# Kernel optimization log

Measured on AMD Instinct MI355X. Metric: run time of the kernel, lower is better.

The kernel has to match this reference:

```python
import jax, jax.numpy as jnp
import numpy as np

B, NPB, F = 8, 8192, 64          # clouds, points/cloud, feature dim
RATIO, R, K, C = 0.25, 0.1, 32, 128
M = int(NPB * RATIO)             # 2048 sampled points per cloud


def setup_inputs() -> dict:
    key = jax.random.key(0)
    k1, k2, k3, k4 = jax.random.split(key, 4)
    x = jax.random.normal(k1, (B * NPB, F), dtype=jnp.float32)
    pos = jax.random.uniform(k2, (B * NPB, 3), dtype=jnp.float32)
    batch = (jnp.arange(B * NPB) // NPB).astype(jnp.int32)
    W1 = jax.random.normal(k3, (F + 3, C), dtype=jnp.float32) * (1.0 / np.sqrt(F + 3))
    b1 = jax.random.normal(k4, (C,), dtype=jnp.float32) * 0.01
    return {"x": x, "pos": pos, "batch": batch, "W1": W1, "b1": b1}


def _fps(pos_b):
    # Farthest point sampling on one cloud [NPB,3] -> [M] indices.
    # Deterministic start at index 0 (random_start=False, eval mode).
    dmin0 = jnp.full((NPB,), jnp.inf, dtype=pos_b.dtype)
    def step(carry, _):
        dmin, last = carry
        d = jnp.sum((pos_b - pos_b[last]) ** 2, axis=-1)
        dmin = jnp.minimum(dmin, d)
        nxt = jnp.argmax(dmin).astype(jnp.int32)
        return (dmin, nxt), last
    (_, _), idx = jax.lax.scan(step, (dmin0, jnp.int32(0)), None, length=M)
    return idx


def reference(x, pos, batch, W1, b1):
    posb = pos.reshape(B, NPB, 3)
    xb = x.reshape(B, NPB, F)

    samp = jax.vmap(_fps)(posb)                                   # [B,M] per-cloud idx
    qpos = jnp.take_along_axis(posb, samp[..., None], axis=1)     # [B,M,3]

    # radius ball query: up to K nearest within R (self always included, d=0)
    d2 = jnp.sum((qpos[:, :, None, :] - posb[:, None, :, :]) ** 2, axis=-1)  # [B,M,NPB]
    score = jnp.where(d2 <= R * R, -d2, -jnp.inf)
    vals, nbr = jax.lax.top_k(score, K)                           # [B,M,K]
    valid = vals > -jnp.inf

    flat = nbr.reshape(B, M * K)
    nbr_pos = jnp.take_along_axis(posb, flat[..., None], axis=1).reshape(B, M, K, 3)
    nbr_x = jnp.take_along_axis(xb, flat[..., None], axis=1).reshape(B, M, K, F)

    # PointNet conv: MLP on [x_j, pos_j - pos_i], max-aggregate over neighbors
    msg_in = jnp.concatenate([nbr_x, nbr_pos - qpos[:, :, None, :]], axis=-1)  # [B,M,K,F+3]
    h = jax.nn.relu(jnp.einsum('bmkf,fc->bmkc', msg_in, W1) + b1)
    h = jnp.where(valid[..., None], h, -jnp.inf)
    out = jnp.max(h, axis=2)                                      # [B,M,C]

    idx_global = (samp + (jnp.arange(B, dtype=jnp.int32) * NPB)[:, None]).reshape(-1)
    return (out.reshape(B * M, C),
            qpos.reshape(B * M, 3),
            jnp.take(batch, idx_global),
            idx_global)
```

## Files before the change

kernel.cpp:

```cpp
#include <hip/hip_runtime.h>

#define NPB 8192
#define NB 8
#define MQ 2048
#define FD 64
#define KN 32
#define CD 128
#define NQ (NB*MQ)
#define CAP 512
#define NCB 248
#define NUNITS (NCB*4)
#define UPC (NUNITS/NB)
#define QITERS ((MQ + UPC - 1) / UPC)
#define PSTRIDE 16

typedef unsigned long long ull;
typedef float v2f __attribute__((ext_vector_type(2)));

#define LDS_BARRIER() asm volatile("s_waitcnt lgkmcnt(0)\n\ts_barrier" ::: "memory")

__device__ __forceinline__ float dist2(float ax, float ay, float az,
                                       float bx, float by, float bz) {
    float dx = __fsub_rn(ax, bx);
    float dy = __fsub_rn(ay, by);
    float dz = __fsub_rn(az, bz);
    return __fadd_rn(__fadd_rn(__fmul_rn(dx, dx), __fmul_rn(dy, dy)), __fmul_rn(dz, dz));
}

__device__ __forceinline__ double key_as_f64(ull k) {
    return __longlong_as_double((long long)k);
}
__device__ __forceinline__ ull key_as_u64(double d) {
    return (ull)__double_as_longlong(d);
}

template <int CTRL>
__device__ __forceinline__ double dpp_max_f64_step(double key) {
    ull u = key_as_u64(key);
    int lo = (int)(unsigned)u, hi = (int)(u >> 32);
    int lo2 = __builtin_amdgcn_update_dpp(0, lo, CTRL, 0xf, 0xf, false);
    int hi2 = __builtin_amdgcn_update_dpp(0, hi, CTRL, 0xf, 0xf, false);
    double o = key_as_f64(((ull)(unsigned)hi2 << 32) | (unsigned)lo2);
    return fmax(key, o);
}

__device__ __forceinline__ double dpp_max_f64(double key) {
    key = dpp_max_f64_step<0x111>(key);
    key = dpp_max_f64_step<0x112>(key);
    key = dpp_max_f64_step<0x114>(key);
    key = dpp_max_f64_step<0x118>(key);
    key = dpp_max_f64_step<0x142>(key);
    key = dpp_max_f64_step<0x143>(key);
    return key;
}

__device__ __forceinline__ double dpp_max_f64_groups8(double key) {
    key = dpp_max_f64_step<0x118>(key);
    key = dpp_max_f64_step<0x142>(key);
    key = dpp_max_f64_step<0x143>(key);
    return key;
}

__device__ __forceinline__ unsigned morton9(float x, float y, float z) {
    unsigned cx = (unsigned)min(7, max(0, (int)(x * 8.0f)));
    unsigned cy = (unsigned)min(7, max(0, (int)(y * 8.0f)));
    unsigned cz = (unsigned)min(7, max(0, (int)(z * 8.0f)));
    return (cx & 1) | ((cy & 1) << 1) | ((cz & 1) << 2)
         | ((cx & 2) << 2) | ((cy & 2) << 3) | ((cz & 2) << 4)
         | ((cx & 4) << 4) | ((cy & 4) << 5) | ((cz & 4) << 6);
}

struct FpsSlot {
    ull key;
    float x, y, z;
    float pad[3];
};
struct FpsSM {
    float2 sxy[NPB];
    float sz[NPB];
    unsigned sidx[NPB];
    __align__(16) FpsSlot slot[2][8];
    unsigned hist[512];
    unsigned off[512];
};
struct UnitSM {
    float msg[KN][68];
    ull buf[CAP];
    int nb[KN];
    int scnt;
    int pad;
};
union SMU {
    FpsSM f;
    UnitSM u[4];
};

__global__ __launch_bounds__(512) void mega_kernel(const float* __restrict__ xin,
                                                   const float* __restrict__ pos,
                                                   const float* __restrict__ W1,
                                                   const float* __restrict__ b1,
                                                   int* __restrict__ samp,
                                                   int* __restrict__ progress,
                                                   float* __restrict__ out) {
    __shared__ SMU sm;
    const int tid = threadIdx.x;

    if (blockIdx.x < NB) {
        const int b = blockIdx.x;
        const int wv = tid >> 6, lane = tid & 63;
        const float* p0 = pos + (size_t)b * NPB * 3;

        sm.f.hist[tid] = 0;
        __syncthreads();
        for (int i = tid; i < NPB; i += 512) {
            float x = p0[i * 3 + 0];
            float y = p0[i * 3 + 1];
            float z = p0[i * 3 + 2];
            sm.f.sxy[i] = make_float2(x, y);
            sm.f.sz[i] = z;
            atomicAdd(&sm.f.hist[morton9(x, y, z)], 1);
        }
        __syncthreads();

        if (tid < 8) {
            FpsSlot* d = &sm.f.slot[1][tid];
            d->key = ((ull)0x7f800000u << 32) | 0xFFFFFFFFu;
            d->x = sm.f.sxy[0].x;
            d->y = sm.f.sxy[0].y;
            d->z = sm.f.sz[0];
        }

        unsigned hval = sm.f.hist[tid];
        unsigned* src = sm.f.hist;
        unsigned* dst = sm.f.off;
        #pragma unroll 1
        for (int d = 1; d < 512; d <<= 1) {
            unsigned v = src[tid];
            if (tid >= d) v += src[tid - d];
            __syncthreads();
            dst[tid] = v;
            __syncthreads();
            unsigned* tmp = src; src = dst; dst = tmp;
        }
        unsigned excl = src[tid] - hval;
        dst[tid] = excl;
        unsigned* cursor = dst;
        __syncthreads();

        for (int i = tid; i < NPB; i += 512) {
            float2 xy = sm.f.sxy[i];
            unsigned m = morton9(xy.x, xy.y, sm.f.sz[i]);
            unsigned p = atomicAdd(&cursor[m], 1);
            sm.f.sidx[p] = (unsigned)i;
        }
        __syncthreads();

        const int perm8[8] = {0, 1, 2, 3, 7, 6, 5, 4};
        const unsigned* sp = &sm.f.sidx[perm8[wv] * 1024 + lane * 16];
        v2f px2[8], py2[8], pz2[8], dmin2[8];
        unsigned norig[16];
        const float inf = __builtin_huge_valf();
        float bx0 = inf, bx1 = -inf;
        float by0 = inf, by1 = -inf;
        float bz0 = inf, bz1 = -inf;
        #pragma unroll
        for (int i = 0; i < 8; i++) {
            unsigned o0 = sp[2 * i + 0];
            unsigned o1 = sp[2 * i + 1];
            norig[2 * i + 0] = ~o0;
            norig[2 * i + 1] = ~o1;
            float2 a = sm.f.sxy[o0], c2 = sm.f.sxy[o1];
            float za = sm.f.sz[o0], zc = sm.f.sz[o1];
            px2[i] = (v2f){a.x, c2.x};
            py2[i] = (v2f){a.y, c2.y};
            pz2[i] = (v2f){za, zc};
            dmin2[i] = (v2f){inf, inf};
            bx0 = fminf(bx0, fminf(a.x, c2.x)); bx1 = fmaxf(bx1, fmaxf(a.x, c2.x));
            by0 = fminf(by0, fminf(a.y, c2.y)); by1 = fmaxf(by1, fmaxf(a.y, c2.y));
            bz0 = fminf(bz0, fminf(za, zc));    bz1 = fmaxf(bz1, fmaxf(za, zc));
        }
        double mykey = key_as_f64((ull)0x7f800000u << 32);
        ull cachedkey = 0;
        float cachedx = 0.f, cachedy = 0.f, cachedz = 0.f;
        __syncthreads();

        for (int t = 0; t < MQ; t++) {
            const FpsSlot* srd = &sm.f.slot[(t - 1) & 1][lane >> 3];
            ulonglong2 rv = *(const ulonglong2*)srd;
            float gzf = srd->z;
            ull kg = rv.x;
            double krd = dpp_max_f64_groups8(key_as_f64(kg));
            ull krb = key_as_u64(krd);
            unsigned whi = (unsigned)__builtin_amdgcn_readlane((int)(krb >> 32), 63);
            unsigned wlo = (unsigned)__builtin_amdgcn_readlane((int)(unsigned)krb, 63);
            ull wk = ((ull)whi << 32) | wlo;
            int last = (int)((~wlo) & (NPB - 1));
            ull iswin = __ballot(kg == wk);
            int wl = __ffsll((long long)iswin) - 1;
            int gxi = (int)(unsigned)rv.y;
            int gyi = (int)(rv.y >> 32);
            float lx = __int_as_float(__builtin_amdgcn_readlane(gxi, wl));
            float ly = __int_as_float(__builtin_amdgcn_readlane(gyi, wl));
            float lz = __int_as_float(__builtin_amdgcn_readlane(__float_as_int(gzf), wl));

            if (tid == 448) {
                samp[b * MQ + t] = last;
                if ((t & 15) == 15)
                    __hip_atomic_store(&progress[b * PSTRIDE], t + 1, __ATOMIC_RELEASE,
                                       __HIP_MEMORY_SCOPE_AGENT);
            }

            float ddx = fmaxf(fmaxf(bx0 - lx, lx - bx1), 0.0f);
            float ddy = fmaxf(fmaxf(by0 - ly, ly - by1), 0.0f);
            float ddz = fmaxf(fmaxf(bz0 - lz, lz - bz1), 0.0f);
            float dlb = ddx * ddx + ddy * ddy + ddz * ddz;
            float cm = __uint_as_float((unsigned)(key_as_u64(mykey) >> 32));
            bool act = __fmul_rn(0.999f, dlb) < cm;

            if (__any(act)) {
                if (act) {
                    #pragma clang fp contract(off)
                    double ba = 0.0, bb = 0.0;
                    #pragma unroll
                    for (int i = 0; i < 8; i++) {
                        v2f dx = px2[i] - lx;
                        v2f dy = py2[i] - ly;
                        v2f dz = pz2[i] - lz;
                        v2f d2v = (dx * dx + dy * dy) + dz * dz;
                        float d0 = fminf(dmin2[i].x, d2v.x);
                        float d1 = fminf(dmin2[i].y, d2v.y);
                        dmin2[i] = (v2f){d0, d1};
                        double k0 = key_as_f64(((ull)__float_as_uint(d0) << 32) | norig[2 * i + 0]);
                        double k1 = key_as_f64(((ull)__float_as_uint(d1) << 32) | norig[2 * i + 1]);
                        ba = fmax(ba, k0);
                        bb = fmax(bb, k1);
                    }
                    mykey = fmax(ba, bb);
                }
                double w = dpp_max_f64(mykey);
                ull wb = key_as_u64(w);
                unsigned chi = (unsigned)__builtin_amdgcn_readlane((int)(wb >> 32), 63);
                unsigned clo = (unsigned)__builtin_amdgcn_readlane((int)(unsigned)wb, 63);
                cachedkey = ((ull)chi << 32) | clo;
                int wi = (int)((~clo) & (NPB - 1));
                float2 cxy = sm.f.sxy[wi];
                cachedx = cxy.x;
                cachedy = cxy.y;
                cachedz = sm.f.sz[wi];
            }
            if (lane == 63) {
                FpsSlot* d = &sm.f.slot[t & 1][wv];
                ulonglong2 wv2;
                wv2.x = cachedkey;
                wv2.y = ((ull)(unsigned)__float_as_int(cachedy) << 32)
                      | (unsigned)__float_as_int(cachedx);
                *(ulonglong2*)d = wv2;
                d->z = cachedz;
            }
            LDS_BARRIER();
        }
        return;
    }

    const int c = blockIdx.x - NB;
    const int unit = tid >> 7;
    const int ut = tid & 127;
    UnitSM& U = sm.u[unit];
    const int g = c * 4 + unit;
    const int b = g & 7;
    const int ui = g >> 3;
    const float RR = (float)(0.1 * 0.1);
    const float* P = pos + (size_t)b * NPB * 3;

    float w[68];
    #pragma unroll
    for (int f = 0; f < 67; f++) w[f] = W1[f * CD + ut];
    w[67] = 0.0f;
    const float bias = b1[ut];

    for (int r = 0; r < QITERS; r++) {
        const int tq = r * UPC + ui;
        const bool active = tq < MQ;
        const int q = (b << 11) + tq;
        int s = 0;
        float qx = 0.f, qy = 0.f, qz = 0.f;

        if (active && ut == 0) {
            while (__hip_atomic_load(&progress[b * PSTRIDE], __ATOMIC_RELAXED,
                                     __HIP_MEMORY_SCOPE_AGENT) < tq + 1) {}
            __builtin_amdgcn_fence(__ATOMIC_ACQUIRE, "agent");
            U.scnt = 0;
        }
        __syncthreads();

        if (active) {
            s = samp[q] & (NPB - 1);
            qx = P[s * 3 + 0]; qy = P[s * 3 + 1]; qz = P[s * 3 + 2];
            for (int p = ut; p < NPB; p += 128) {
                float xx = P[p * 3 + 0];
                float yy = P[p * 3 + 1];
                float zz = P[p * 3 + 2];
                float d2v = dist2(qx, qy, qz, xx, yy, zz);
                if (d2v <= RR) {
                    int slot = atomicAdd(&U.scnt, 1);
                    if (slot < CAP)
                        U.buf[slot] = ((ull)__float_as_uint(d2v) << 32) | (unsigned)p;
                }
            }
        }
        __syncthreads();

        int n = 0, nk = 0;
        if (active) {
            n = U.scnt; if (n > CAP) n = CAP;
            nk = (n < KN) ? n : KN;
        }
        if (active && ut < 64) {
            if (n <= 64) {
                ull key = (ut < n) ? U.buf[ut] : ~0ULL;
                #pragma unroll
                for (int k = 2; k <= 64; k <<= 1) {
                    #pragma unroll
                    for (int j = k >> 1; j > 0; j >>= 1) {
                        ull o = __shfl_xor(key, (unsigned)j, 64);
                        bool ascending = ((ut & k) == 0);
                        bool upper = ((ut & j) != 0);
                        bool keepMin = (ascending != upper);
                        ull mn = (o < key) ? o : key;
                        ull mx = (o < key) ? key : o;
                        key = keepMin ? mn : mx;
                    }
                }
                if (ut < nk) U.nb[ut] = ((int)(unsigned)key) & (NPB - 1);
            } else {
                ull ck[CAP / 64];
                #pragma unroll
                for (int i = 0; i < CAP / 64; i++) {
                    int sl = ut + i * 64;
                    ck[i] = (sl < n) ? U.buf[sl] : ~0ULL;
                }
                for (int rr = 0; rr < nk; rr++) {
                    ull lm = ck[0];
                    int li = 0;
                    #pragma unroll
                    for (int i = 1; i < CAP / 64; i++) {
                        if (ck[i] < lm) { lm = ck[i]; li = i; }
                    }
                    ull gm = lm;
                    #pragma unroll
                    for (int off = 1; off < 64; off <<= 1) {
                        ull o = __shfl_xor(gm, off, 64);
                        gm = (o < gm) ? o : gm;
                    }
                    ull won = __ballot(lm == gm);
                    int wlane = __ffsll((long long)won) - 1;
                    if (ut == wlane) ck[li] = ~0ULL;
                    if (ut == 0) U.nb[rr] = ((int)(unsigned)gm) & (NPB - 1);
                }
            }
        }
        __syncthreads();

        if (active) {
            const int lane64 = ut & 63, half = ut >> 6;
            for (int k = half; k < nk; k += 2) {
                int p = U.nb[k];
                U.msg[k][lane64] = xin[((size_t)(b * NPB + p)) * FD + lane64];
            }
            if (ut < nk) {
                int p = U.nb[ut];
                U.msg[ut][64] = __fsub_rn(P[p * 3 + 0], qx);
                U.msg[ut][65] = __fsub_rn(P[p * 3 + 1], qy);
                U.msg[ut][66] = __fsub_rn(P[p * 3 + 2], qz);
                U.msg[ut][67] = 0.0f;
            }
        }
        __syncthreads();

        if (active) {
            float acc = 0.0f;
            for (int k = 0; k < nk; k++) {
                float s0 = 0.f, s1 = 0.f, s2 = 0.f, s3 = 0.f;
                #pragma unroll
                for (int f4 = 0; f4 < 17; f4++) {
                    float4 mv = *(const float4*)&U.msg[k][f4 * 4];
                    s0 = fmaf(mv.x, w[f4 * 4 + 0], s0);
                    s1 = fmaf(mv.y, w[f4 * 4 + 1], s1);
                    s2 = fmaf(mv.z, w[f4 * 4 + 2], s2);
                    s3 = fmaf(mv.w, w[f4 * 4 + 3], s3);
                }
                float h = (s0 + s1) + (s2 + s3) + bias;
                h = fmaxf(h, 0.0f);
                acc = fmaxf(acc, h);
            }
            out[(size_t)q * CD + ut] = acc;
            if (ut == 0) {
                float* qp = out + (size_t)NQ * CD;
                qp[q * 3 + 0] = qx;
                qp[q * 3 + 1] = qy;
                qp[q * 3 + 2] = qz;
                float* bo = qp + (size_t)NQ * 3;
                bo[q] = (float)b;
                float* io = bo + NQ;
                io[q] = (float)(b * NPB + s);
            }
        }
    }
}

extern "C" void kernel_launch(void* const* d_in, const int* in_sizes, int n_in,
                              void* d_out, int out_size, void* d_ws, size_t ws_size,
                              hipStream_t stream) {
    const float* x   = (const float*)d_in[0];
    const float* pos = (const float*)d_in[1];
    const float* W1  = (const float*)d_in[3];
    const float* b1  = (const float*)d_in[4];
    float* out = (float*)d_out;

    int* samp = (int*)d_ws;
    int* progress = samp + NQ;

    hipMemsetAsync(progress, 0, NB * PSTRIDE * sizeof(int), stream);
    mega_kernel<<<NB + NCB, 512, 0, stream>>>(x, pos, W1, b1, samp, progress, out);
}
```

Before: 1.505 ms.

## Double block size to 1024 threads so FPS spreads points over 16 waves

Each FPS block now runs 16 waves of 1024 threads, so each lane holds 8 points instead of 16 and the per-step distance update is shorter. The cross-wave reduction now reads 16 slots with a 4-lane DPP group, and the neighbor-query blocks pack 8 units per block over half as many blocks. The wave-wide argmax reduction is also skipped when no lane's key changed. The costs are more waves taking part in each per-iteration barrier, and launch bounds of 1024 threads, which may cap registers for the 68-float weight array in the unit path.

```diff
diff --git a/kernel.cpp b/kernel.cpp
--- a/kernel.cpp
+++ b/kernel.cpp
@@ -8,8 +8,8 @@
 #define CD 128
 #define NQ (NB*MQ)
 #define CAP 512
-#define NCB 248
-#define NUNITS (NCB*4)
+#define NCB 124
+#define NUNITS (NCB*8)
 #define UPC (NUNITS/NB)
 #define QITERS ((MQ + UPC - 1) / UPC)
 #define PSTRIDE 16
@@ -54,7 +54,8 @@
     return key;
 }
 
-__device__ __forceinline__ double dpp_max_f64_groups8(double key) {
+__device__ __forceinline__ double dpp_max_f64_groups4(double key) {
+    key = dpp_max_f64_step<0x114>(key);
     key = dpp_max_f64_step<0x118>(key);
     key = dpp_max_f64_step<0x142>(key);
     key = dpp_max_f64_step<0x143>(key);
@@ -70,16 +71,16 @@
          | ((cx & 4) << 4) | ((cy & 4) << 5) | ((cz & 4) << 6);
 }
 
-struct FpsSlot {
+struct __align__(16) FpsSlot {
     ull key;
     float x, y, z;
-    float pad[3];
+    float pad[7];
 };
 struct FpsSM {
     float2 sxy[NPB];
     float sz[NPB];
     unsigned sidx[NPB];
-    __align__(16) FpsSlot slot[2][8];
+    FpsSlot slot[2][16];
     unsigned hist[512];
     unsigned off[512];
 };
@@ -92,16 +93,16 @@
 };
 union SMU {
     FpsSM f;
-    UnitSM u[4];
+    UnitSM u[8];
 };
 
-__global__ __launch_bounds__(512) void mega_kernel(const float* __restrict__ xin,
-                                                   const float* __restrict__ pos,
-                                                   const float* __restrict__ W1,
-                                                   const float* __restrict__ b1,
-                                                   int* __restrict__ samp,
-                                                   int* __restrict__ progress,
-                                                   float* __restrict__ out) {
+__global__ __launch_bounds__(1024, 4) void mega_kernel(const float* __restrict__ xin,
+                                                       const float* __restrict__ pos,
+                                                       const float* __restrict__ W1,
+                                                       const float* __restrict__ b1,
+                                                       int* __restrict__ samp,
+                                                       int* __restrict__ progress,
+                                                       float* __restrict__ out) {
     __shared__ SMU sm;
     const int tid = threadIdx.x;
 
@@ -110,9 +111,9 @@
         const int wv = tid >> 6, lane = tid & 63;
         const float* p0 = pos + (size_t)b * NPB * 3;
 
-        sm.f.hist[tid] = 0;
-        __syncthreads();
-        for (int i = tid; i < NPB; i += 512) {
+        if (tid < 512) sm.f.hist[tid] = 0;
+        __syncthreads();
+        for (int i = tid; i < NPB; i += 1024) {
             float x = p0[i * 3 + 0];
             float y = p0[i * 3 + 1];
             float z = p0[i * 3 + 2];
@@ -122,7 +123,7 @@
         }
         __syncthreads();
 
-        if (tid < 8) {
+        if (tid < 16) {
             FpsSlot* d = &sm.f.slot[1][tid];
             d->key = ((ull)0x7f800000u << 32) | 0xFFFFFFFFu;
             d->x = sm.f.sxy[0].x;
@@ -130,24 +131,26 @@
             d->z = sm.f.sz[0];
         }
 
-        unsigned hval = sm.f.hist[tid];
+        unsigned hval = (tid < 512) ? sm.f.hist[tid] : 0u;
         unsigned* src = sm.f.hist;
         unsigned* dst = sm.f.off;
         #pragma unroll 1
         for (int d = 1; d < 512; d <<= 1) {
-            unsigned v = src[tid];
-            if (tid >= d) v += src[tid - d];
+            unsigned v = 0;
+            if (tid < 512) {
+                v = src[tid];
+                if (tid >= d) v += src[tid - d];
+            }
             __syncthreads();
-            dst[tid] = v;
+            if (tid < 512) dst[tid] = v;
             __syncthreads();
             unsigned* tmp = src; src = dst; dst = tmp;
         }
-        unsigned excl = src[tid] - hval;
-        dst[tid] = excl;
+        if (tid < 512) dst[tid] = src[tid] - hval;
         unsigned* cursor = dst;
         __syncthreads();
 
-        for (int i = tid; i < NPB; i += 512) {
+        for (int i = tid; i < NPB; i += 1024) {
             float2 xy = sm.f.sxy[i];
             unsigned m = morton9(xy.x, xy.y, sm.f.sz[i]);
             unsigned p = atomicAdd(&cursor[m], 1);
@@ -155,16 +158,16 @@
         }
         __syncthreads();
 
-        const int perm8[8] = {0, 1, 2, 3, 7, 6, 5, 4};
-        const unsigned* sp = &sm.f.sidx[perm8[wv] * 1024 + lane * 16];
-        v2f px2[8], py2[8], pz2[8], dmin2[8];
-        unsigned norig[16];
+        const int region = (wv * 5) & 15;
+        const unsigned* sp = &sm.f.sidx[region * 512 + lane * 8];
+        v2f px2[4], py2[4], pz2[4], dmin2[4];
+        unsigned norig[8];
         const float inf = __builtin_huge_valf();
         float bx0 = inf, bx1 = -inf;
         float by0 = inf, by1 = -inf;
         float bz0 = inf, bz1 = -inf;
         #pragma unroll
-        for (int i = 0; i < 8; i++) {
+        for (int i = 0; i < 4; i++) {
             unsigned o0 = sp[2 * i + 0];
             unsigned o1 = sp[2 * i + 1];
             norig[2 * i + 0] = ~o0;
@@ -185,11 +188,11 @@
         __syncthreads();
 
         for (int t = 0; t < MQ; t++) {
-            const FpsSlot* srd = &sm.f.slot[(t - 1) & 1][lane >> 3];
+            const FpsSlot* srd = &sm.f.slot[(t - 1) & 1][lane >> 2];
             ulonglong2 rv = *(const ulonglong2*)srd;
             float gzf = srd->z;
             ull kg = rv.x;
-            double krd = dpp_max_f64_groups8(key_as_f64(kg));
+            double krd = dpp_max_f64_groups4(key_as_f64(kg));
             ull krb = key_as_u64(krd);
             unsigned whi = (unsigned)__builtin_amdgcn_readlane((int)(krb >> 32), 63);
             unsigned wlo = (unsigned)__builtin_amdgcn_readlane((int)(unsigned)krb, 63);
@@ -203,7 +206,7 @@
             float ly = __int_as_float(__builtin_amdgcn_readlane(gyi, wl));
             float lz = __int_as_float(__builtin_amdgcn_readlane(__float_as_int(gzf), wl));
 
-            if (tid == 448) {
+            if (tid == 960) {
                 samp[b * MQ + t] = last;
                 if ((t & 15) == 15)
                     __hip_atomic_store(&progress[b * PSTRIDE], t + 1, __ATOMIC_RELEASE,
@@ -218,11 +221,12 @@
             bool act = __fmul_rn(0.999f, dlb) < cm;
 
             if (__any(act)) {
+                double oldkey = mykey;
                 if (act) {
                     #pragma clang fp contract(off)
                     double ba = 0.0, bb = 0.0;
                     #pragma unroll
-                    for (int i = 0; i < 8; i++) {
+                    for (int i = 0; i < 4; i++) {
                         v2f dx = px2[i] - lx;
                         v2f dy = py2[i] - ly;
                         v2f dz = pz2[i] - lz;
@@ -237,16 +241,18 @@
                     }
                     mykey = fmax(ba, bb);
                 }
-                double w = dpp_max_f64(mykey);
-                ull wb = key_as_u64(w);
-                unsigned chi = (unsigned)__builtin_amdgcn_readlane((int)(wb >> 32), 63);
-                unsigned clo = (unsigned)__builtin_amdgcn_readlane((int)(unsigned)wb, 63);
-                cachedkey = ((ull)chi << 32) | clo;
-                int wi = (int)((~clo) & (NPB - 1));
-                float2 cxy = sm.f.sxy[wi];
-                cachedx = cxy.x;
-                cachedy = cxy.y;
-                cachedz = sm.f.sz[wi];
+                if (!__all(mykey == oldkey)) {
+                    double w = dpp_max_f64(mykey);
+                    ull wb = key_as_u64(w);
+                    unsigned chi = (unsigned)__builtin_amdgcn_readlane((int)(wb >> 32), 63);
+                    unsigned clo = (unsigned)__builtin_amdgcn_readlane((int)(unsigned)wb, 63);
+                    cachedkey = ((ull)chi << 32) | clo;
+                    int wi = (int)((~clo) & (NPB - 1));
+                    float2 cxy = sm.f.sxy[wi];
+                    cachedx = cxy.x;
+                    cachedy = cxy.y;
+                    cachedz = sm.f.sz[wi];
+                }
             }
             if (lane == 63) {
                 FpsSlot* d = &sm.f.slot[t & 1][wv];
@@ -266,7 +272,7 @@
     const int unit = tid >> 7;
     const int ut = tid & 127;
     UnitSM& U = sm.u[unit];
-    const int g = c * 4 + unit;
+    const int g = c * 8 + unit;
     const int b = g & 7;
     const int ui = g >> 3;
     const float RR = (float)(0.1 * 0.1);
@@ -421,5 +427,5 @@
     int* progress = samp + NQ;
 
     hipMemsetAsync(progress, 0, NB * PSTRIDE * sizeof(int), stream);
-    mega_kernel<<<NB + NCB, 512, 0, stream>>>(x, pos, W1, b1, samp, progress, out);
-}
+    mega_kernel<<<NB + NCB, 1024, 0, stream>>>(x, pos, W1, b1, samp, progress, out);
+}
```

Measured after the change: 2.867 ms. 1.9x slower.

## Split FPS lane points into two Morton sub-boxes with independent pruning

Applied to the files above, without the earlier changes.

Each lane in the FPS loop now holds two groups of 8 points from opposite ends of the Morton order, each with its own bounding box and running max key. Each group is recomputed only when its own bound check passes, and the wave-wide DPP reduction and LDS coordinate fetch are skipped when no lane's combined key changed. The goal is to shorten the serial per-iteration critical path. The cost is extra registers and two ballots per step, and pairing segments 15-wv with wv may weaken locality within a lane.

```diff
diff --git a/kernel.cpp b/kernel.cpp
--- a/kernel.cpp
+++ b/kernel.cpp
@@ -155,18 +155,17 @@
         }
         __syncthreads();
 
-        const int perm8[8] = {0, 1, 2, 3, 7, 6, 5, 4};
-        const unsigned* sp = &sm.f.sidx[perm8[wv] * 1024 + lane * 16];
+        const unsigned* sp0 = &sm.f.sidx[wv * 512 + lane * 8];
+        const unsigned* sp1 = &sm.f.sidx[(15 - wv) * 512 + lane * 8];
         v2f px2[8], py2[8], pz2[8], dmin2[8];
         unsigned norig[16];
         const float inf = __builtin_huge_valf();
-        float bx0 = inf, bx1 = -inf;
-        float by0 = inf, by1 = -inf;
-        float bz0 = inf, bz1 = -inf;
+        float ax0 = inf, ax1 = -inf, ay0 = inf, ay1 = -inf, az0 = inf, az1 = -inf;
+        float ex0 = inf, ex1 = -inf, ey0 = inf, ey1 = -inf, ez0 = inf, ez1 = -inf;
         #pragma unroll
-        for (int i = 0; i < 8; i++) {
-            unsigned o0 = sp[2 * i + 0];
-            unsigned o1 = sp[2 * i + 1];
+        for (int i = 0; i < 4; i++) {
+            unsigned o0 = sp0[2 * i + 0];
+            unsigned o1 = sp0[2 * i + 1];
             norig[2 * i + 0] = ~o0;
             norig[2 * i + 1] = ~o1;
             float2 a = sm.f.sxy[o0], c2 = sm.f.sxy[o1];
@@ -175,11 +174,28 @@
             py2[i] = (v2f){a.y, c2.y};
             pz2[i] = (v2f){za, zc};
             dmin2[i] = (v2f){inf, inf};
-            bx0 = fminf(bx0, fminf(a.x, c2.x)); bx1 = fmaxf(bx1, fmaxf(a.x, c2.x));
-            by0 = fminf(by0, fminf(a.y, c2.y)); by1 = fmaxf(by1, fmaxf(a.y, c2.y));
-            bz0 = fminf(bz0, fminf(za, zc));    bz1 = fmaxf(bz1, fmaxf(za, zc));
-        }
-        double mykey = key_as_f64((ull)0x7f800000u << 32);
+            ax0 = fminf(ax0, fminf(a.x, c2.x)); ax1 = fmaxf(ax1, fmaxf(a.x, c2.x));
+            ay0 = fminf(ay0, fminf(a.y, c2.y)); ay1 = fmaxf(ay1, fmaxf(a.y, c2.y));
+            az0 = fminf(az0, fminf(za, zc));    az1 = fmaxf(az1, fmaxf(za, zc));
+        }
+        #pragma unroll
+        for (int i = 0; i < 4; i++) {
+            unsigned o0 = sp1[2 * i + 0];
+            unsigned o1 = sp1[2 * i + 1];
+            norig[8 + 2 * i + 0] = ~o0;
+            norig[8 + 2 * i + 1] = ~o1;
+            float2 a = sm.f.sxy[o0], c2 = sm.f.sxy[o1];
+            float za = sm.f.sz[o0], zc = sm.f.sz[o1];
+            px2[4 + i] = (v2f){a.x, c2.x};
+            py2[4 + i] = (v2f){a.y, c2.y};
+            pz2[4 + i] = (v2f){za, zc};
+            dmin2[4 + i] = (v2f){inf, inf};
+            ex0 = fminf(ex0, fminf(a.x, c2.x)); ex1 = fmaxf(ex1, fmaxf(a.x, c2.x));
+            ey0 = fminf(ey0, fminf(a.y, c2.y)); ey1 = fmaxf(ey1, fmaxf(a.y, c2.y));
+            ez0 = fminf(ez0, fminf(za, zc));    ez1 = fmaxf(ez1, fmaxf(za, zc));
+        }
+        double mykey0 = key_as_f64((ull)0x7f800000u << 32);
+        double mykey1 = mykey0;
         ull cachedkey = 0;
         float cachedx = 0.f, cachedy = 0.f, cachedz = 0.f;
         __syncthreads();
@@ -210,19 +226,28 @@
                                        __HIP_MEMORY_SCOPE_AGENT);
             }
 
-            float ddx = fmaxf(fmaxf(bx0 - lx, lx - bx1), 0.0f);
-            float ddy = fmaxf(fmaxf(by0 - ly, ly - by1), 0.0f);
-            float ddz = fmaxf(fmaxf(bz0 - lz, lz - bz1), 0.0f);
-            float dlb = ddx * ddx + ddy * ddy + ddz * ddz;
-            float cm = __uint_as_float((unsigned)(key_as_u64(mykey) >> 32));
-            bool act = __fmul_rn(0.999f, dlb) < cm;
-
-            if (__any(act)) {
-                if (act) {
+            float d0x = fmaxf(fmaxf(ax0 - lx, lx - ax1), 0.0f);
+            float d0y = fmaxf(fmaxf(ay0 - ly, ly - ay1), 0.0f);
+            float d0z = fmaxf(fmaxf(az0 - lz, lz - az1), 0.0f);
+            float dlb0 = d0x * d0x + d0y * d0y + d0z * d0z;
+            float d1x = fmaxf(fmaxf(ex0 - lx, lx - ex1), 0.0f);
+            float d1y = fmaxf(fmaxf(ey0 - ly, ly - ey1), 0.0f);
+            float d1z = fmaxf(fmaxf(ez0 - lz, lz - ez1), 0.0f);
+            float dlb1 = d1x * d1x + d1y * d1y + d1z * d1z;
+            float cm0 = __uint_as_float((unsigned)(key_as_u64(mykey0) >> 32));
+            float cm1 = __uint_as_float((unsigned)(key_as_u64(mykey1) >> 32));
+            bool act0 = __fmul_rn(0.999f, dlb0) < cm0;
+            bool act1 = __fmul_rn(0.999f, dlb1) < cm1;
+            bool wa0 = __any(act0);
+            bool wa1 = __any(act1);
+
+            if (wa0 || wa1) {
+                double oldc = fmax(mykey0, mykey1);
+                if (wa0 && act0) {
                     #pragma clang fp contract(off)
                     double ba = 0.0, bb = 0.0;
                     #pragma unroll
-                    for (int i = 0; i < 8; i++) {
+                    for (int i = 0; i < 4; i++) {
                         v2f dx = px2[i] - lx;
                         v2f dy = py2[i] - ly;
                         v2f dz = pz2[i] - lz;
@@ -235,18 +260,40 @@
                         ba = fmax(ba, k0);
                         bb = fmax(bb, k1);
                     }
-                    mykey = fmax(ba, bb);
-                }
-                double w = dpp_max_f64(mykey);
-                ull wb = key_as_u64(w);
-                unsigned chi = (unsigned)__builtin_amdgcn_readlane((int)(wb >> 32), 63);
-                unsigned clo = (unsigned)__builtin_amdgcn_readlane((int)(unsigned)wb, 63);
-                cachedkey = ((ull)chi << 32) | clo;
-                int wi = (int)((~clo) & (NPB - 1));
-                float2 cxy = sm.f.sxy[wi];
-                cachedx = cxy.x;
-                cachedy = cxy.y;
-                cachedz = sm.f.sz[wi];
+                    mykey0 = fmax(ba, bb);
+                }
+                if (wa1 && act1) {
+                    #pragma clang fp contract(off)
+                    double ba = 0.0, bb = 0.0;
+                    #pragma unroll
+                    for (int i = 4; i < 8; i++) {
+                        v2f dx = px2[i] - lx;
+                        v2f dy = py2[i] - ly;
+                        v2f dz = pz2[i] - lz;
+                        v2f d2v = (dx * dx + dy * dy) + dz * dz;
+                        float d0 = fminf(dmin2[i].x, d2v.x);
+                        float d1 = fminf(dmin2[i].y, d2v.y);
+                        dmin2[i] = (v2f){d0, d1};
+                        double k0 = key_as_f64(((ull)__float_as_uint(d0) << 32) | norig[2 * i + 0]);
+                        double k1 = key_as_f64(((ull)__float_as_uint(d1) << 32) | norig[2 * i + 1]);
+                        ba = fmax(ba, k0);
+                        bb = fmax(bb, k1);
+                    }
+                    mykey1 = fmax(ba, bb);
+                }
+                double comb = fmax(mykey0, mykey1);
+                if (!__all(comb == oldc)) {
+                    double w = dpp_max_f64(comb);
+                    ull wb = key_as_u64(w);
+                    unsigned chi = (unsigned)__builtin_amdgcn_readlane((int)(wb >> 32), 63);
+                    unsigned clo = (unsigned)__builtin_amdgcn_readlane((int)(unsigned)wb, 63);
+                    cachedkey = ((ull)chi << 32) | clo;
+                    int wi = (int)((~clo) & (NPB - 1));
+                    float2 cxy = sm.f.sxy[wi];
+                    cachedx = cxy.x;
+                    cachedy = cxy.y;
+                    cachedz = sm.f.sz[wi];
+                }
             }
             if (lane == 63) {
                 FpsSlot* d = &sm.f.slot[t & 1][wv];
```

New measurement: 1.521 ms. No clear change (+1.1%).
